# Kernel tuning notes

Measured on AMD Instinct MI355X. Metric: run time of the kernel, lower is better.

Reference implementation:

```python
import jax, jax.numpy as jnp
import numpy as np

PS = 32768        # bag size (num patches)
D_IN = 1024       # input feature dim (hardcoded Linear(1024,512))
D = 512           # mlp_dim
D_ATT = 128       # DAttention hidden dim (ABMIL D)
N_CLS = 2
MASK_RATIO_H = 0.5
K_MASK = int(np.ceil(PS * MASK_RATIO_H))   # high-attention patches masked out
LEN_KEEP = PS - K_MASK                     # static keep length


def setup_inputs() -> dict:
    key = jax.random.key(0)
    ks = jax.random.split(key, 8)
    n = lambda i, shp, sc: jax.random.normal(ks[i], shp, dtype=jnp.float32) * sc
    return {
        "x": n(0, (1, PS, D_IN), 1.0),
        "attn": jax.random.uniform(ks[1], (1, PS), dtype=jnp.float32),
        "teacher_cls_feat": n(2, (1, D), 1.0),
        # patch_to_emb: Linear(1024,512) + ReLU (xavier-ish init)
        "W_emb": n(3, (D_IN, D), 0.03), "b_emb": jnp.zeros((D,), jnp.float32),
        # DAttention score net: Linear(512,128) -> GELU -> Linear(128,1)
        "W_a1": n(4, (D, D_ATT), 0.06), "b_a1": jnp.zeros((D_ATT,), jnp.float32),
        "W_a2": n(5, (D_ATT, 1), 0.12), "b_a2": jnp.zeros((1,), jnp.float32),
        # predictor: Linear(512, n_classes)
        "W_pred": n(6, (D, N_CLS), 0.06), "b_pred": jnp.zeros((N_CLS,), jnp.float32),
    }


def _keep_ids(attn_1d):
    # select_mask_fn(largest=True, mask_ratio=0.5, random_ratio=1.0, select_inv=False):
    # top-k highest-attention indices are MASKED; keep = set-difference complement.
    _, top_idx = jax.lax.top_k(attn_1d, K_MASK)
    masked = jnp.zeros((PS,), dtype=bool).at[top_idx].set(True)
    # complement in ascending order (matches set(range(ps)).difference iteration)
    return jnp.nonzero(~masked, size=LEN_KEEP, fill_value=0)[0]


def reference(x, attn, teacher_cls_feat, W_emb, b_emb, W_a1, b_a1, W_a2, b_a2,
              W_pred, b_pred):
    # patch_to_emb + ReLU  (dropout=0 -> identity)
    h = jax.nn.relu(jnp.einsum("bnd,de->bne", x, W_emb) + b_emb)   # [1,PS,512]

    keep = _keep_ids(attn[0])                                        # [LEN_KEEP]
    hk = h[:, keep, :]                                               # [1,LK,512]

    # DAttention pooling: scores -> softmax over kept instances -> weighted sum
    s = jax.nn.gelu(jnp.einsum("bnd,dk->bnk", hk, W_a1) + b_a1, approximate=False)
    s = (jnp.einsum("bnk,ko->bno", s, W_a2) + b_a2)[..., 0]          # [1,LK]
    A = jax.nn.softmax(s, axis=-1)
    feat = jnp.einsum("bn,bnd->bd", A, hk)                           # [1,512]

    logit = feat @ W_pred + b_pred                                   # [1,2]

    # SoftTargetCrossEntropy_v2 between student bag feature and (detached) teacher
    t = jax.lax.stop_gradient(teacher_cls_feat)
    cls_loss = jnp.mean(jnp.sum(
        -jax.nn.softmax(t, axis=-1) * jax.nn.log_softmax(feat, axis=-1), axis=-1))

    return logit, cls_loss
```

## Files before the change

kernel.cpp:

```cpp
#include <hip/hip_runtime.h>
#include <hip/hip_bf16.h>
#include <math.h>

#define PS    32768
#define DIN   1024
#define DMID  512
#define DATT  128
#define KMASK 16384
#define LKEEP 16384

typedef unsigned short u16;
typedef __attribute__((ext_vector_type(8))) short short8;
typedef __attribute__((ext_vector_type(4))) float f32x4;

__device__ __forceinline__ u16 f2bf(float f){
  unsigned x = __float_as_uint(f);
  unsigned r = (x + 0x7fffu + ((x >> 16) & 1u)) >> 16;
  return (u16)r;
}
__device__ __forceinline__ u16 f2bf_hw(float f){
  __hip_bfloat16 h = __float2bfloat16(f);
  return *reinterpret_cast<u16*>(&h);
}
__device__ __forceinline__ float bf2f(u16 u){
  return __uint_as_float(((unsigned)u) << 16);
}
__device__ __forceinline__ unsigned fkey(float f){
  unsigned b = __float_as_uint(f);
  return (b & 0x80000000u) ? ~b : (b | 0x80000000u);
}

#define GLDS16(g,l) __builtin_amdgcn_global_load_lds( \
    (const __attribute__((address_space(1))) void*)(g), \
    (__attribute__((address_space(3))) void*)(l), 16, 0, 0)

__global__ __launch_bounds__(1024) void k_head(const float* __restrict__ attn,
                                               int* __restrict__ keep_ids,
                                               const float* __restrict__ Wemb,
                                               u16* __restrict__ wet,
                                               const float* __restrict__ Wa1,
                                               u16* __restrict__ wa1t){
  __shared__ int histL[16384];
  __shared__ int suf[1024];
  __shared__ unsigned ck[4096];
  __shared__ int ci[4096];
  __shared__ float tile[4][32][33];
  __shared__ int sh_B, sh_kp, cnt;
  __shared__ unsigned sh_C;
  __shared__ int sh_thr;
  __shared__ int wbase[16];
  __shared__ int sh_base;
  const int t = threadIdx.x, b = blockIdx.x;

  if (b >= 32){
    const int grp = t >> 8, ts = t & 255;
    const int ob = (b - 32) * 4 + grp;
    const int tx = ts & 31, ty = ts >> 5;
    if (ob < 512){
      const int c0 = (ob & 15) * 32, r0 = (ob >> 4) * 32;
      for (int i = 0; i < 32; i += 8)
        tile[grp][ty + i][tx] = Wemb[(size_t)(r0 + ty + i) * DMID + c0 + tx];
      __syncthreads();
      for (int i = 0; i < 32; i += 8)
        wet[(size_t)(c0 + ty + i) * DIN + r0 + tx] = f2bf(tile[grp][tx][ty + i]);
    } else {
      const int b2 = ob - 512;
      const int c0 = (b2 & 3) * 32, r0 = (b2 >> 2) * 32;
      for (int i = 0; i < 32; i += 8)
        tile[grp][ty + i][tx] = Wa1[(size_t)(r0 + ty + i) * DATT + c0 + tx];
      __syncthreads();
      for (int i = 0; i < 32; i += 8)
        wa1t[(size_t)(c0 + ty + i) * DMID + r0 + tx] = f2bf(tile[grp][tx][ty + i]);
    }
    return;
  }

  for (int i = t; i < 16384; i += 1024) histL[i] = 0;
  __syncthreads();
  for (int i = t; i < PS; i += 1024)
    atomicAdd(&histL[fkey(attn[i]) >> 18], 1);
  __syncthreads();

  int local[16]; int s = 0;
  const int base = t * 16;
  for (int j = 0; j < 16; j++){ local[j] = histL[base + j]; s += local[j]; }
  suf[t] = s; __syncthreads();
  for (int off = 1; off < 1024; off <<= 1){
    int v = (t + off < 1024) ? suf[t + off] : 0;
    __syncthreads();
    suf[t] += v;
    __syncthreads();
  }
  const int above = (t < 1023) ? suf[t + 1] : 0;
  if (above < KMASK && KMASK <= suf[t]){
    int cum = above;
    for (int bb = 15; bb >= 0; bb--){
      int c = local[bb];
      if (cum + c >= KMASK){ sh_B = base + bb; sh_kp = KMASK - cum; break; }
      cum += c;
    }
  }
  if (t == 0) cnt = 0;
  __syncthreads();
  const unsigned B = (unsigned)sh_B;
  const int kp = sh_kp;

  for (int i = t; i < PS; i += 1024){
    unsigned u = fkey(attn[i]);
    if ((u >> 18) == B){
      int p = atomicAdd(&cnt, 1);
      if (p < 4096){ ck[p] = u; ci[p] = i; }
    }
  }
  __syncthreads();
  int n = cnt; if (n > 4096) n = 4096;
  for (int p = t; p < n; p += 1024){
    const unsigned mk = ck[p]; const int mi = ci[p];
    int rank = 0;
    for (int j = 0; j < n; j++){
      const unsigned kj = ck[j];
      rank += (kj > mk) || (kj == mk && ci[j] < mi);
    }
    if (rank == kp - 1){ sh_C = mk; sh_thr = mi; }
  }
  __syncthreads();
  const unsigned C = sh_C;
  const int thr = sh_thr;

  const int i = b * 1024 + t;
  const unsigned u = fkey(attn[i]);
  const bool kept = (u < C) || (u == C && i > thr);
  const unsigned long long bal = __ballot(kept);
  const int lane = t & 63, w = t >> 6;
  if (lane == 0) wbase[w] = __popcll(bal);
  int cnt2 = 0;
  for (int j = t; j < b * 1024; j += 1024){
    const unsigned u2 = fkey(attn[j]);
    cnt2 += (u2 < C) || (u2 == C && j > thr);
  }
  suf[t] = cnt2; __syncthreads();
  for (int st = 512; st > 0; st >>= 1){ if (t < st) suf[t] += suf[t + st]; __syncthreads(); }
  if (t == 0){
    sh_base = suf[0];
    int run = 0;
    for (int j = 0; j < 16; j++){ int c = wbase[j]; wbase[j] = run; run += c; }
  }
  __syncthreads();
  if (kept){
    const int lr = __popcll(bal & ((1ull << lane) - 1ull));
    keep_ids[sh_base + wbase[w] + lr] = i;
  }
}

__global__ __launch_bounds__(512) void k_gemm1g(const float* __restrict__ xg,
                                                const int* __restrict__ keep,
                                                const u16* __restrict__ wet,
                                                const float* __restrict__ bemb,
                                                u16* __restrict__ hbf){
  __shared__ __align__(16) u16 As[128 * 32];
  __shared__ __align__(16) u16 Bs[128 * 32];
  const int t = threadIdx.x;
  const int wid = t >> 6, lane = t & 63;
  const int g = lane >> 4, li = lane & 15;
  const int m_ = blockIdx.x;
  const int by = (m_ & 7) + 8 * (m_ >> 5);
  const int bx = (m_ >> 3) & 3;
  const int brow = by * 128, bcol = bx * 128;
  const int wrow0 = (wid >> 2) * 64, wcol0 = (wid & 3) * 32;

  f32x4 acc[4][2];
  for (int mm = 0; mm < 4; mm++)
    for (int nn = 0; nn < 2; nn++)
      acc[mm][nn] = (f32x4){0.f, 0.f, 0.f, 0.f};

  const int rsub = t >> 2, q8 = (t & 3) * 8;
  const float* gA = xg + (size_t)keep[brow + rsub] * DIN + q8;
  const int r4 = lane >> 2, cB = lane & 3;
  const u16* gB = wet + ((size_t)(bcol + wid * 16 + r4) * DIN + cB * 8);
  u16* lB = Bs + wid * 512;

  for (int k0 = 0; k0 < DIN; k0 += 32){
    float4 avlo = *(const float4*)(gA + k0);
    float4 avhi = *(const float4*)(gA + k0 + 4);
    GLDS16(gB + k0, lB);
    {
      short8 pk;
      pk[0] = (short)f2bf_hw(avlo.x); pk[1] = (short)f2bf_hw(avlo.y);
      pk[2] = (short)f2bf_hw(avlo.z); pk[3] = (short)f2bf_hw(avlo.w);
      pk[4] = (short)f2bf_hw(avhi.x); pk[5] = (short)f2bf_hw(avhi.y);
      pk[6] = (short)f2bf_hw(avhi.z); pk[7] = (short)f2bf_hw(avhi.w);
      *(short8*)&As[rsub * 32 + q8] = pk;
    }
    __syncthreads();
    short8 a[4], b[2];
#pragma unroll
    for (int mm = 0; mm < 4; mm++)
      a[mm] = *(const short8*)&As[(wrow0 + mm * 16 + li) * 32 + g * 8];
#pragma unroll
    for (int nn = 0; nn < 2; nn++)
      b[nn] = *(const short8*)&Bs[(wcol0 + nn * 16 + li) * 32 + g * 8];
    for (int mm = 0; mm < 4; mm++)
      for (int nn = 0; nn < 2; nn++)
        acc[mm][nn] = __builtin_amdgcn_mfma_f32_16x16x32_bf16(a[mm], b[nn], acc[mm][nn], 0, 0, 0);
    __syncthreads();
  }

  for (int nn = 0; nn < 2; nn++){
    const int col = bcol + wcol0 + nn * 16 + li;
    const float be = bemb[col];
    for (int mm = 0; mm < 4; mm++){
      const int row0 = brow + wrow0 + mm * 16 + g * 4;
      f32x4 v = acc[mm][nn];
      for (int r = 0; r < 4; r++){
        float val = v[r] + be;
        if (val < 0.f) val = 0.f;
        hbf[(size_t)(row0 + r) * DMID + col] = f2bf(val);
      }
    }
  }
}

__global__ __launch_bounds__(256) void k_gemm2(const u16* __restrict__ hbf,
                                               const u16* __restrict__ wa1t,
                                               const float* __restrict__ ba1,
                                               const float* __restrict__ wa2,
                                               const float* __restrict__ ba2,
                                               float* __restrict__ s_out,
                                               float* __restrict__ smax,
                                               float* __restrict__ ssum,
                                               float* __restrict__ partial){
  __shared__ __align__(16) u16 As[64 * 32];
  __shared__ __align__(16) u16 Bs[128 * 32];
  __shared__ float p_lds[64];
  __shared__ float sh_m;
  const int t = threadIdx.x;
  const int wid = t >> 6, lane = t & 63;
  const int g = lane >> 4, li = lane & 15;
  const int brow = blockIdx.x * 64;
  const int wrow0 = (wid >> 1) * 32, wcol0 = (wid & 1) * 64;

  f32x4 acc[2][4];
  for (int m = 0; m < 2; m++)
    for (int n = 0; n < 4; n++)
      acc[m][n] = (f32x4){0.f, 0.f, 0.f, 0.f};

  const int r4 = lane >> 2, c4 = lane & 3;
  const u16* gA = hbf  + ((size_t)(brow + wid * 16 + r4) * DMID + c4 * 8);
  const u16* gB = wa1t + ((size_t)(wid * 32 + r4) * DMID + c4 * 8);
  u16* lA = As + wid * 512;
  u16* lB = Bs + wid * 1024;

  for (int k0 = 0; k0 < DMID; k0 += 32){
    GLDS16(gA + k0,             lA);
    GLDS16(gB + k0,             lB);
    GLDS16(gB + 16 * DMID + k0, lB + 512);
    __syncthreads();
    short8 a[2], b[4];
    for (int m = 0; m < 2; m++)
      a[m] = *(const short8*)&As[(wrow0 + m * 16 + li) * 32 + g * 8];
    for (int n = 0; n < 4; n++)
      b[n] = *(const short8*)&Bs[(wcol0 + n * 16 + li) * 32 + g * 8];
    for (int m = 0; m < 2; m++)
      for (int n = 0; n < 4; n++)
        acc[m][n] = __builtin_amdgcn_mfma_f32_16x16x32_bf16(a[m], b[n], acc[m][n], 0, 0, 0);
    __syncthreads();
  }

  float rsum[2][4] = {{0.f,0.f,0.f,0.f},{0.f,0.f,0.f,0.f}};
  for (int n = 0; n < 4; n++){
    const int col = wcol0 + n * 16 + li;
    const float b1 = ba1[col], w2 = wa2[col];
    for (int m = 0; m < 2; m++){
      f32x4 v = acc[m][n];
      for (int r = 0; r < 4; r++){
        float xv = v[r] + b1;
        float ge = 0.5f * xv * (1.0f + erff(xv * 0.70710678118654752f));
        rsum[m][r] += ge * w2;
      }
    }
  }
  const float bb = ba2[0];
  for (int m = 0; m < 2; m++){
    for (int r = 0; r < 4; r++){
      float v = rsum[m][r];
      v += __shfl_xor(v, 1); v += __shfl_xor(v, 2);
      v += __shfl_xor(v, 4); v += __shfl_xor(v, 8);
      if (li == 0) s_out[brow + wrow0 + m * 16 + g * 4 + r] = v + bb;
    }
  }
  __syncthreads();
  if (t < 64){
    const float sv = s_out[brow + t];
    float mx = sv;
    for (int off = 1; off < 64; off <<= 1) mx = fmaxf(mx, __shfl_xor(mx, off));
    float ez = expf(sv - mx);
    for (int off = 1; off < 64; off <<= 1) ez += __shfl_xor(ez, off);
    if (t == 0){ smax[blockIdx.x] = mx; ssum[blockIdx.x] = ez; sh_m = mx; }
  }
  __syncthreads();
  if (t < 64) p_lds[t] = expf(s_out[brow + t] - sh_m);
  __syncthreads();
  {
    const int d0 = t * 2;
    float v0 = 0.f, v1 = 0.f;
    for (int j = 0; j < 64; j++){
      const float pj = p_lds[j];
      const unsigned hv = *(const unsigned*)&hbf[(size_t)(brow + j) * DMID + d0];
      v0 += pj * bf2f((u16)(hv & 0xffffu));
      v1 += pj * bf2f((u16)(hv >> 16));
    }
    partial[(size_t)blockIdx.x * DMID + d0]     = v0;
    partial[(size_t)blockIdx.x * DMID + d0 + 1] = v1;
  }
}

__global__ __launch_bounds__(512) void k_final(const float* __restrict__ partial,
                                               const float* __restrict__ smax,
                                               const float* __restrict__ ssum,
                                               const float* __restrict__ teach,
                                               const float* __restrict__ Wp,
                                               const float* __restrict__ bp,
                                               float* __restrict__ out){
  __shared__ float red[512];
  __shared__ float coef[256];
  const int t = threadIdx.x;

  red[t] = (t < 256) ? smax[t] : -INFINITY; __syncthreads();
  for (int st = 256; st > 0; st >>= 1){ if (t < st) red[t] = fmaxf(red[t], red[t + st]); __syncthreads(); }
  const float m_s = red[0]; __syncthreads();
  if (t < 256) coef[t] = expf(smax[t] - m_s);
  __syncthreads();
  red[t] = (t < 256) ? ssum[t] * coef[t] : 0.f; __syncthreads();
  for (int st = 256; st > 0; st >>= 1){ if (t < st) red[t] += red[t + st]; __syncthreads(); }
  const float invZ = 1.0f / red[0]; __syncthreads();

  float f = 0.f;
  for (int b = 0; b < 256; b++) f += partial[(size_t)b * DMID + t] * coef[b];
  f *= invZ;
  const float td = teach[t];

  red[t] = f; __syncthreads();
  for (int st = 256; st > 0; st >>= 1){ if (t < st) red[t] = fmaxf(red[t], red[t + st]); __syncthreads(); }
  const float mf = red[0]; __syncthreads();

  red[t] = td; __syncthreads();
  for (int st = 256; st > 0; st >>= 1){ if (t < st) red[t] = fmaxf(red[t], red[t + st]); __syncthreads(); }
  const float mt = red[0]; __syncthreads();

  red[t] = expf(f - mf); __syncthreads();
  for (int st = 256; st > 0; st >>= 1){ if (t < st) red[t] += red[t + st]; __syncthreads(); }
  const float Zf = red[0]; __syncthreads();

  const float pt = expf(td - mt);
  red[t] = pt; __syncthreads();
  for (int st = 256; st > 0; st >>= 1){ if (t < st) red[t] += red[t + st]; __syncthreads(); }
  const float Zt = red[0]; __syncthreads();

  red[t] = pt * f; __syncthreads();
  for (int st = 256; st > 0; st >>= 1){ if (t < st) red[t] += red[t + st]; __syncthreads(); }
  const float S1 = red[0]; __syncthreads();

  red[t] = f * Wp[t * 2 + 0]; __syncthreads();
  for (int st = 256; st > 0; st >>= 1){ if (t < st) red[t] += red[t + st]; __syncthreads(); }
  const float L0 = red[0]; __syncthreads();

  red[t] = f * Wp[t * 2 + 1]; __syncthreads();
  for (int st = 256; st > 0; st >>= 1){ if (t < st) red[t] += red[t + st]; __syncthreads(); }
  const float L1 = red[0];

  if (t == 0){
    out[0] = L0 + bp[0];
    out[1] = L1 + bp[1];
    out[2] = (mf + logf(Zf)) - S1 / Zt;
  }
}

extern "C" void kernel_launch(void* const* d_in, const int* in_sizes, int n_in,
                              void* d_out, int out_size, void* d_ws, size_t ws_size,
                              hipStream_t stream){
  const float* x     = (const float*)d_in[0];
  const float* attn  = (const float*)d_in[1];
  const float* teach = (const float*)d_in[2];
  const float* Wemb  = (const float*)d_in[3];
  const float* bemb  = (const float*)d_in[4];
  const float* Wa1   = (const float*)d_in[5];
  const float* ba1   = (const float*)d_in[6];
  const float* Wa2   = (const float*)d_in[7];
  const float* ba2   = (const float*)d_in[8];
  const float* Wp    = (const float*)d_in[9];
  const float* bp    = (const float*)d_in[10];
  float* out = (float*)d_out;

  char* ws = (char*)d_ws;
  int*   keep = (int*)(ws + 0);
  float* s    = (float*)(ws + 65536);
  float* smax = (float*)(ws + 131072);
  float* ssum = (float*)(ws + 132096);
  u16*   wet  = (u16*)(ws + 200704);
  u16*   wa1t = (u16*)(ws + 200704 + 1048576);
  float* partial = (float*)(ws + 200704 + 1048576 + 131072);
  u16*   hbf  = (u16*)(ws + 200704 + 1048576 + 131072 + 33554432);

  k_head<<<dim3(176), dim3(1024), 0, stream>>>(attn, keep, Wemb, wet, Wa1, wa1t);
  k_gemm1g<<<dim3(512), dim3(512), 0, stream>>>(x, keep, wet, bemb, hbf);
  k_gemm2<<<dim3(LKEEP / 64), dim3(256), 0, stream>>>(hbf, wa1t, ba1, Wa2, ba2, s, smax, ssum, partial);
  k_final<<<dim3(1), dim3(512), 0, stream>>>(partial, smax, ssum, teach, Wp, bp, out);
}
```

Measured before the change: 110.0 us.

## Double-buffer LDS tiles and software-pipeline gathered loads in first GEMM

The gather-GEMM kernel now uses two LDS buffers for A and B. It prefetches the B tile one step ahead via global_load_lds and the fp32 A rows two steps ahead in registers. Manual s_waitcnt counts and a single barrier per iteration replace the two __syncthreads, so global-load latency overlaps with the MFMA work. The cost is double the LDS footprint and fragile hand-counted vmcnt values that must match the compiler's instruction ordering.

```diff
diff --git a/kernel.cpp b/kernel.cpp
--- a/kernel.cpp
+++ b/kernel.cpp
@@ -33,6 +33,8 @@
 #define GLDS16(g,l) __builtin_amdgcn_global_load_lds( \
     (const __attribute__((address_space(1))) void*)(g), \
     (__attribute__((address_space(3))) void*)(l), 16, 0, 0)
+
+#define MEMPIN() asm volatile("" ::: "memory")
 
 __global__ __launch_bounds__(1024) void k_head(const float* __restrict__ attn,
                                                int* __restrict__ keep_ids,
@@ -157,8 +159,8 @@
                                                 const u16* __restrict__ wet,
                                                 const float* __restrict__ bemb,
                                                 u16* __restrict__ hbf){
-  __shared__ __align__(16) u16 As[128 * 32];
-  __shared__ __align__(16) u16 Bs[128 * 32];
+  __shared__ __align__(16) u16 As[2][128 * 32];
+  __shared__ __align__(16) u16 Bs[2][128 * 32];
   const int t = threadIdx.x;
   const int wid = t >> 6, lane = t & 63;
   const int g = lane >> 4, li = lane & 15;
@@ -177,33 +179,69 @@
   const float* gA = xg + (size_t)keep[brow + rsub] * DIN + q8;
   const int r4 = lane >> 2, cB = lane & 3;
   const u16* gB = wet + ((size_t)(bcol + wid * 16 + r4) * DIN + cB * 8);
-  u16* lB = Bs + wid * 512;
-
-  for (int k0 = 0; k0 < DIN; k0 += 32){
-    float4 avlo = *(const float4*)(gA + k0);
-    float4 avhi = *(const float4*)(gA + k0 + 4);
-    GLDS16(gB + k0, lB);
-    {
-      short8 pk;
-      pk[0] = (short)f2bf_hw(avlo.x); pk[1] = (short)f2bf_hw(avlo.y);
-      pk[2] = (short)f2bf_hw(avlo.z); pk[3] = (short)f2bf_hw(avlo.w);
-      pk[4] = (short)f2bf_hw(avhi.x); pk[5] = (short)f2bf_hw(avhi.y);
-      pk[6] = (short)f2bf_hw(avhi.z); pk[7] = (short)f2bf_hw(avhi.w);
-      *(short8*)&As[rsub * 32 + q8] = pk;
-    }
-    __syncthreads();
-    short8 a[4], b[2];
-#pragma unroll
-    for (int mm = 0; mm < 4; mm++)
-      a[mm] = *(const short8*)&As[(wrow0 + mm * 16 + li) * 32 + g * 8];
-#pragma unroll
-    for (int nn = 0; nn < 2; nn++)
-      b[nn] = *(const short8*)&Bs[(wcol0 + nn * 16 + li) * 32 + g * 8];
-    for (int mm = 0; mm < 4; mm++)
-      for (int nn = 0; nn < 2; nn++)
-        acc[mm][nn] = __builtin_amdgcn_mfma_f32_16x16x32_bf16(a[mm], b[nn], acc[mm][nn], 0, 0, 0);
-    __syncthreads();
-  }
+
+#define CVT_STORE(dstbuf, lo, hi) { \
+    short8 pk_; \
+    pk_[0] = (short)f2bf_hw((lo).x); pk_[1] = (short)f2bf_hw((lo).y); \
+    pk_[2] = (short)f2bf_hw((lo).z); pk_[3] = (short)f2bf_hw((lo).w); \
+    pk_[4] = (short)f2bf_hw((hi).x); pk_[5] = (short)f2bf_hw((hi).y); \
+    pk_[6] = (short)f2bf_hw((hi).z); pk_[7] = (short)f2bf_hw((hi).w); \
+    *(short8*)&As[dstbuf][rsub * 32 + q8] = pk_; }
+
+#define READ_MFMA(cur) { \
+    short8 a_[4], b_[2]; \
+    _Pragma("unroll") \
+    for (int mm = 0; mm < 4; mm++) \
+      a_[mm] = *(const short8*)&As[cur][(wrow0 + mm * 16 + li) * 32 + g * 8]; \
+    _Pragma("unroll") \
+    for (int nn = 0; nn < 2; nn++) \
+      b_[nn] = *(const short8*)&Bs[cur][(wcol0 + nn * 16 + li) * 32 + g * 8]; \
+    for (int mm = 0; mm < 4; mm++) \
+      for (int nn = 0; nn < 2; nn++) \
+        acc[mm][nn] = __builtin_amdgcn_mfma_f32_16x16x32_bf16(a_[mm], b_[nn], acc[mm][nn], 0, 0, 0); }
+
+  float4 a0lo = *(const float4*)(gA);
+  float4 a0hi = *(const float4*)(gA + 4);
+  MEMPIN();
+  GLDS16(gB, &Bs[0][wid * 512]);
+  MEMPIN();
+  float4 avlo = *(const float4*)(gA + 32);
+  float4 avhi = *(const float4*)(gA + 36);
+  MEMPIN();
+  CVT_STORE(0, a0lo, a0hi);
+  asm volatile("s_waitcnt vmcnt(2) lgkmcnt(0)" ::: "memory");
+  __builtin_amdgcn_s_barrier();
+
+#pragma unroll 2
+  for (int k = 0; k < 30; k++){
+    const int cur = k & 1, nxt = cur ^ 1;
+    GLDS16(gB + (k + 1) * 32, &Bs[nxt][wid * 512]);
+    MEMPIN();
+    float4 nvlo = *(const float4*)(gA + (k + 2) * 32);
+    float4 nvhi = *(const float4*)(gA + (k + 2) * 32 + 4);
+    asm volatile("s_waitcnt vmcnt(5)" ::: "memory");
+    READ_MFMA(cur);
+    MEMPIN();
+    CVT_STORE(nxt, avlo, avhi);
+    avlo = nvlo; avhi = nvhi;
+    asm volatile("s_waitcnt lgkmcnt(0)" ::: "memory");
+    __builtin_amdgcn_s_barrier();
+  }
+  {
+    GLDS16(gB + 31 * 32, &Bs[1][wid * 512]);
+    asm volatile("s_waitcnt vmcnt(3)" ::: "memory");
+    READ_MFMA(0);
+    MEMPIN();
+    CVT_STORE(1, avlo, avhi);
+    asm volatile("s_waitcnt lgkmcnt(0)" ::: "memory");
+    __builtin_amdgcn_s_barrier();
+  }
+  {
+    asm volatile("s_waitcnt vmcnt(0)" ::: "memory");
+    READ_MFMA(1);
+  }
+#undef CVT_STORE
+#undef READ_MFMA
 
   for (int nn = 0; nn < 2; nn++){
     const int col = bcol + wcol0 + nn * 16 + li;
```

Result: faster. 107.6 us, median of 2 (-2.2%).
